# Kernel optimization log

Hardware: AMD Instinct MI355X
Metric: run time of the kernel (lower is better)

Reference implementation:

```python
import jax, jax.numpy as jnp
import numpy as np

MODEL_DIM = 1024
NUM_HEADS = 16
K_DIM = MODEL_DIM // NUM_HEADS


def setup_inputs() -> dict:
    key = jax.random.key(0)
    k1, k2, k3 = jax.random.split(key, 3)
    x = jax.random.normal(k1, (4, 2048, MODEL_DIM), dtype=jnp.float32)
    # nn.Linear(model_dim, 3*model_dim, bias=False): store as [D, 3D] so y = x @ W
    wqkv = jax.random.normal(k2, (MODEL_DIM, 3 * MODEL_DIM), dtype=jnp.float32) * (MODEL_DIM ** -0.5)
    wo = jax.random.normal(k3, (MODEL_DIM, MODEL_DIM), dtype=jnp.float32) * (MODEL_DIM ** -0.5)
    return {"x": x, "wqkv": wqkv, "wo": wo}


def reference(x, wqkv, wo):
    B, L, D = x.shape
    H, K = NUM_HEADS, K_DIM
    qkv = jnp.einsum("bld,de->ble", x, wqkv)  # [B, L, 3D]
    q, k, v = jnp.split(qkv, 3, axis=-1)
    # Faithful to source: plain reshape (no transpose) into [B, H, L, K]
    qh = q.reshape(B, H, L, K)
    kh = k.reshape(B, H, L, K)
    vh = v.reshape(B, H, L, K)
    scores = jnp.einsum("bhlk,bhmk->bhlm", qh, kh) / jnp.sqrt(jnp.float32(K))
    # Faithful quirk: softmax over dim=1 (head axis), as in the source
    probs = jax.nn.softmax(scores, axis=1)
    attended = jnp.einsum("bhlm,bhmk->bhlk", probs, vh)  # [B, H, L, K]
    concatted = attended.transpose(0, 2, 1, 3).reshape(B, L, D)
    return jnp.einsum("bld,de->ble", concatted, wo)
```

## Files before the change

### kernel.cpp

```cpp
#include <hip/hip_runtime.h>
#include <hip/hip_bf16.h>
#include <stdint.h>

typedef __attribute__((ext_vector_type(8))) short short8;
typedef __attribute__((ext_vector_type(4))) float floatx4;

#define QSCALE 0.18033688f

__device__ __forceinline__ unsigned short f2bf(float f) {
    unsigned int u = __float_as_uint(f);
    u += 0x7fffu + ((u >> 16) & 1u);
    return (unsigned short)(u >> 16);
}
__device__ __forceinline__ unsigned int pack2bf(float a, float b) {
    __hip_bfloat162 h = __float22bfloat162_rn(make_float2(a, b));
    return *reinterpret_cast<unsigned int*>(&h);
}

__device__ __forceinline__ void async16(const void* g, void* l) {
    __builtin_amdgcn_global_load_lds(
        (const __attribute__((address_space(1))) unsigned int*)g,
        (__attribute__((address_space(3))) unsigned int*)l, 16, 0, 0);
}

__global__ __launch_bounds__(256) void cvt_bf16(const float* __restrict__ src,
                                                unsigned short* __restrict__ dst, int n8) {
    int i = blockIdx.x * 256 + threadIdx.x;
    if (i >= n8) return;
    const float4 a = ((const float4*)src)[2 * i];
    const float4 b = ((const float4*)src)[2 * i + 1];
    ushort4 lo, hi;
    lo.x = f2bf(a.x); lo.y = f2bf(a.y); lo.z = f2bf(a.z); lo.w = f2bf(a.w);
    hi.x = f2bf(b.x); hi.y = f2bf(b.y); hi.z = f2bf(b.z); hi.w = f2bf(b.w);
    ((ushort4*)dst)[2 * i] = lo;
    ((ushort4*)dst)[2 * i + 1] = hi;
}

__global__ __launch_bounds__(256) void tcvt(const float* __restrict__ src,
                                            unsigned short* __restrict__ dst, int R, int C) {
    __shared__ unsigned short t[64][72];
    const int tid = threadIdx.x;
    const int r0 = blockIdx.y * 64, c0 = blockIdx.x * 64;
    #pragma unroll
    for (int it = 0; it < 4; it++) {
        int idx = it * 256 + tid;
        int rr = idx >> 4, cc = (idx & 15) * 4;
        float4 v = *(const float4*)(src + (size_t)(r0 + rr) * C + c0 + cc);
        t[cc + 0][rr] = f2bf(v.x);
        t[cc + 1][rr] = f2bf(v.y);
        t[cc + 2][rr] = f2bf(v.z);
        t[cc + 3][rr] = f2bf(v.w);
    }
    __syncthreads();
    #pragma unroll
    for (int it = 0; it < 2; it++) {
        int idx = it * 256 + tid;
        int cc = idx >> 3, r8 = (idx & 7) * 8;
        short8 v = *(const short8*)&t[cc][r8];
        *(short8*)(dst + (size_t)(c0 + cc) * R + r0 + r8) = v;
    }
}

__global__ __launch_bounds__(256) void vtrans(const unsigned short* __restrict__ vb,
                                              unsigned short* __restrict__ vbt) {
    __shared__ unsigned short t[64][72];
    const int tid = threadIdx.x;
    const int bh = blockIdx.y, m0 = blockIdx.x * 64;
    const unsigned short* src = vb + ((size_t)bh * 2048 + m0) * 64;
    unsigned short* dst = vbt + ((size_t)bh << 17) + m0;
    union { short8 v; unsigned short u[8]; } tmp;
    #pragma unroll
    for (int it = 0; it < 2; it++) {
        int idx = it * 256 + tid;
        int m = idx >> 3, c8 = (idx & 7) * 8;
        tmp.v = *(const short8*)(src + (size_t)m * 64 + c8);
        #pragma unroll
        for (int j = 0; j < 8; j++) t[c8 + j][m] = tmp.u[j];
    }
    __syncthreads();
    #pragma unroll
    for (int it = 0; it < 2; it++) {
        int idx = it * 256 + tid;
        int k = idx >> 3, c8 = (idx & 7) * 8;
        short8 v = *(const short8*)&t[k][c8];
        *(short8*)(dst + (size_t)k * 2048 + c8) = v;
    }
}

__global__ __launch_bounds__(256) void qkv_gemm(
    const unsigned short* __restrict__ A, const unsigned short* __restrict__ Bt,
    unsigned short* __restrict__ qb, unsigned short* __restrict__ kb,
    unsigned short* __restrict__ vb)
{
    __shared__ __align__(16) unsigned short As[128 * 32];
    __shared__ __align__(16) unsigned short Bs[128 * 32];
    const int tid = threadIdx.x, wave = tid >> 6, lane = tid & 63;
    const int quad = lane >> 4, lr = lane & 15;
    const int wr = wave >> 1, wc = wave & 1;
    const int bm = blockIdx.y * 128, bn = blockIdx.x * 128;
    const int lrow = lane >> 2, lcol = (lane & 3) * 8;

    floatx4 acc[4][4];
    #pragma unroll
    for (int i = 0; i < 4; i++)
        #pragma unroll
        for (int j = 0; j < 4; j++) acc[i][j] = (floatx4)0.0f;

    for (int k0 = 0; k0 < 1024; k0 += 32) {
        #pragma unroll
        for (int t = 0; t < 2; t++) {
            const int rbase = wave * 32 + t * 16;
            const int r = rbase + lrow;
            async16(A  + (size_t)(bm + r) * 1024 + k0 + lcol, &As[rbase * 32]);
            async16(Bt + (size_t)(bn + r) * 1024 + k0 + lcol, &Bs[rbase * 32]);
        }
        __syncthreads();
        short8 af[4], bfr[4];
        #pragma unroll
        for (int i = 0; i < 4; i++)
            af[i] = *(const short8*)&As[(wr * 64 + i * 16 + lr) * 32 + quad * 8];
        #pragma unroll
        for (int j = 0; j < 4; j++)
            bfr[j] = *(const short8*)&Bs[(wc * 64 + j * 16 + lr) * 32 + quad * 8];
        #pragma unroll
        for (int i = 0; i < 4; i++)
            #pragma unroll
            for (int j = 0; j < 4; j++)
                acc[i][j] = __builtin_amdgcn_mfma_f32_16x16x32_bf16(af[i], bfr[j], acc[i][j], 0, 0, 0);
        __syncthreads();
    }

    const int part = bn >> 10;
    unsigned short* __restrict__ dstb = (part == 0) ? qb : ((part == 1) ? kb : vb);
    const float sc = (part == 0) ? QSCALE : 1.0f;
    const int dbase = bn & 1023;
    #pragma unroll
    for (int i = 0; i < 4; i++)
        #pragma unroll
        for (int j = 0; j < 4; j++)
            #pragma unroll
            for (int r = 0; r < 4; r++) {
                int row = bm + wr * 64 + i * 16 + quad * 4 + r;
                int d   = dbase + wc * 64 + j * 16 + lr;
                int b = row >> 11, l = row & 2047;
                int flat = (l << 10) | d;
                int h = flat >> 17;
                int rem = flat & 131071;
                int l2 = rem >> 6, kk = rem & 63;
                dstb[((size_t)(b * 16 + h) * 2048 + l2) * 64 + kk] = f2bf(acc[i][j][r] * sc);
            }
}

__global__ __launch_bounds__(256) void out_gemm(
    const unsigned short* __restrict__ A, const unsigned short* __restrict__ Bt,
    float* __restrict__ C)
{
    __shared__ __align__(16) unsigned short As[128 * 32];
    __shared__ __align__(16) unsigned short Bs[128 * 32];
    const int tid = threadIdx.x, wave = tid >> 6, lane = tid & 63;
    const int quad = lane >> 4, lr = lane & 15;
    const int wr = wave >> 1, wc = wave & 1;
    const int bm = blockIdx.y * 128, bn = blockIdx.x * 128;
    const int lrow = lane >> 2, lcol = (lane & 3) * 8;

    floatx4 acc[4][4];
    #pragma unroll
    for (int i = 0; i < 4; i++)
        #pragma unroll
        for (int j = 0; j < 4; j++) acc[i][j] = (floatx4)0.0f;

    for (int k0 = 0; k0 < 1024; k0 += 32) {
        #pragma unroll
        for (int t = 0; t < 2; t++) {
            const int rbase = wave * 32 + t * 16;
            const int r = rbase + lrow;
            async16(A  + (size_t)(bm + r) * 1024 + k0 + lcol, &As[rbase * 32]);
            async16(Bt + (size_t)(bn + r) * 1024 + k0 + lcol, &Bs[rbase * 32]);
        }
        __syncthreads();
        short8 af[4], bfr[4];
        #pragma unroll
        for (int i = 0; i < 4; i++)
            af[i] = *(const short8*)&As[(wr * 64 + i * 16 + lr) * 32 + quad * 8];
        #pragma unroll
        for (int j = 0; j < 4; j++)
            bfr[j] = *(const short8*)&Bs[(wc * 64 + j * 16 + lr) * 32 + quad * 8];
        #pragma unroll
        for (int i = 0; i < 4; i++)
            #pragma unroll
            for (int j = 0; j < 4; j++)
                acc[i][j] = __builtin_amdgcn_mfma_f32_16x16x32_bf16(af[i], bfr[j], acc[i][j], 0, 0, 0);
        __syncthreads();
    }
    #pragma unroll
    for (int i = 0; i < 4; i++)
        #pragma unroll
        for (int j = 0; j < 4; j++)
            #pragma unroll
            for (int r = 0; r < 4; r++) {
                int row = bm + wr * 64 + i * 16 + quad * 4 + r;
                int col = bn + wc * 64 + j * 16 + lr;
                C[(size_t)row * 1024 + col] = acc[i][j][r];
            }
}

__global__ __launch_bounds__(256, 5) void attn_denom(
    const unsigned short* __restrict__ qb, const unsigned short* __restrict__ kb,
    unsigned short* __restrict__ drpT)
{
    __shared__ __align__(16) unsigned short Qs[2][64 * 64];
    __shared__ __align__(16) unsigned short Ks[2][64 * 64];
    const int tid = threadIdx.x, wave = tid >> 6, lane = tid & 63;
    const int quad = lane >> 4, lr = lane & 15;
    const int e7 = lr & 7;
    const int M0 = blockIdx.x * 64, L0 = blockIdx.y * 64, b = blockIdx.z;

    const int klr = lane >> 3;
    const int ksw8 = ((lane & 7) ^ klr) * 8;
    const size_t hb0 = ((size_t)(b * 16)) << 17;
    const unsigned short* qsrc0 = qb + hb0 + (size_t)(L0 + wave * 8 + klr) * 64 + ksw8;
    const unsigned short* ksrc0 = kb + hb0 + (size_t)(M0 + wave * 8 + klr) * 64 + ksw8;

    floatx4 e[4];
    #pragma unroll
    for (int i = 0; i < 4; i++) e[i] = (floatx4)0.0f;

    async16(qsrc0,           &Qs[0][(wave * 8) * 64]);
    async16(qsrc0 + 32 * 64, &Qs[0][(32 + wave * 8) * 64]);
    async16(ksrc0,           &Ks[0][(wave * 8) * 64]);
    async16(ksrc0 + 32 * 64, &Ks[0][(32 + wave * 8) * 64]);
    __syncthreads();

    for (int h = 0; h < 16; h++) {
        const int cur = h & 1, nxt = cur ^ 1;
        if (h < 15) {
            const unsigned short* qs = qsrc0 + ((size_t)(h + 1) << 17);
            const unsigned short* ks = ksrc0 + ((size_t)(h + 1) << 17);
            async16(qs,           &Qs[nxt][(wave * 8) * 64]);
            async16(qs + 32 * 64, &Qs[nxt][(32 + wave * 8) * 64]);
            async16(ks,           &Ks[nxt][(wave * 8) * 64]);
            async16(ks + 32 * 64, &Ks[nxt][(32 + wave * 8) * 64]);
        }
        const unsigned short* qsp = &Qs[cur][0];
        const unsigned short* ksp = &Ks[cur][0];
        const int rq = wave * 16 + lr;
        short8 qf0 = *(const short8*)&qsp[rq * 64 + (quad ^ e7) * 8];
        short8 qf1 = *(const short8*)&qsp[rq * 64 + ((4 + quad) ^ e7) * 8];
        #pragma unroll
        for (int mt = 0; mt < 4; mt++) {
            const int rk = mt * 16 + lr;
            short8 kf0 = *(const short8*)&ksp[rk * 64 + (quad ^ e7) * 8];
            short8 kf1 = *(const short8*)&ksp[rk * 64 + ((4 + quad) ^ e7) * 8];
            floatx4 s = (floatx4)0.0f;
            __builtin_amdgcn_s_setprio(1);
            s = __builtin_amdgcn_mfma_f32_16x16x32_bf16(kf0, qf0, s, 0, 0, 0);
            s = __builtin_amdgcn_mfma_f32_16x16x32_bf16(kf1, qf1, s, 0, 0, 0);
            __builtin_amdgcn_s_setprio(0);
            e[mt][0] += __builtin_amdgcn_exp2f(s[0]);
            e[mt][1] += __builtin_amdgcn_exp2f(s[1]);
            e[mt][2] += __builtin_amdgcn_exp2f(s[2]);
            e[mt][3] += __builtin_amdgcn_exp2f(s[3]);
        }
        if (h < 15) __syncthreads();
    }
    #pragma unroll
    for (int mt = 0; mt < 4; mt++) {
        float r0 = __builtin_amdgcn_rcpf(e[mt][0]);
        float r1 = __builtin_amdgcn_rcpf(e[mt][1]);
        float r2 = __builtin_amdgcn_rcpf(e[mt][2]);
        float r3 = __builtin_amdgcn_rcpf(e[mt][3]);
        uint2 o;
        o.x = pack2bf(r0, r1);
        o.y = pack2bf(r2, r3);
        int mtg = (M0 >> 4) + mt;
        int ltg = (L0 >> 4) + wave;
        *(uint2*)(drpT + ((((size_t)b * 128 + mtg) * 128 + ltg) << 8) + lane * 4) = o;
    }
}

__global__ __launch_bounds__(256, 4) void attn_pv(
    const unsigned short* __restrict__ qb, const unsigned short* __restrict__ kb,
    const unsigned short* __restrict__ vbt, const unsigned short* __restrict__ drpT,
    unsigned short* __restrict__ cb)
{
    __shared__ __align__(16) unsigned short KV[3][64 * 64];
    __shared__ __align__(16) unsigned short Ps[128 * 64];
    const int tid = threadIdx.x, wave = tid >> 6, lane = tid & 63;
    const int quad = lane >> 4, lr = lane & 15;
    const int e7 = lr & 7;
    const int flat = blockIdx.x;
    const int swz = (flat & 7) * 128 + (flat >> 3);
    const int Lt = swz & 15;
    const int h = (swz >> 4) & 15;
    const int b = swz >> 8;
    const int L0 = Lt * 128;
    const size_t head = (size_t)(b * 16 + h);
    const unsigned short* qbase = qb + (head << 17);
    const unsigned short* kbase = kb + (head << 17);
    const unsigned short* vtb   = vbt + (head << 17);
    const unsigned short* dbase = drpT + (((size_t)b * 128 * 128 + (L0 >> 4) + wave * 2) << 8) + lane * 4;

    const int klr = lane >> 3;
    const int ksw = (lane & 7) ^ klr;
    const unsigned short* ksrc0 = kbase + (size_t)(wave * 8 + klr) * 64 + ksw * 8;
    const unsigned short* vsrc0 = vtb + (size_t)(wave * 8 + klr) * 2048 + ksw * 8;

    short8 qf[2][2];
    #pragma unroll
    for (int j = 0; j < 2; j++) {
        const unsigned short* qr = qbase + (size_t)(L0 + wave * 32 + j * 16 + lr) * 64;
        qf[j][0] = *(const short8*)(qr + quad * 8);
        qf[j][1] = *(const short8*)(qr + 32 + quad * 8);
    }

    floatx4 oacc[2][4];
    #pragma unroll
    for (int i = 0; i < 2; i++)
        #pragma unroll
        for (int j = 0; j < 4; j++) oacc[i][j] = (floatx4)0.0f;

    async16(ksrc0,             &KV[0][(wave * 8) * 64]);
    async16(ksrc0 + 32 * 64,   &KV[0][(32 + wave * 8) * 64]);
    async16(vsrc0,             &KV[1][(wave * 8) * 64]);
    async16(vsrc0 + 32 * 2048, &KV[1][(32 + wave * 8) * 64]);
    uint2 du[4][2];
    #pragma unroll
    for (int mt = 0; mt < 4; mt++)
        #pragma unroll
        for (int j = 0; j < 2; j++)
            du[mt][j] = *(const uint2*)(dbase + ((size_t)mt << 15) + (j << 8));
    __syncthreads();

    int kcur = 0, vcur = 1, sp = 2;
    for (int t = 0; t < 32; t++) {
        const int M0 = t * 64;
        if (t < 31) {
            const unsigned short* ks = ksrc0 + (size_t)(M0 + 64) * 64;
            async16(ks,           &KV[sp][(wave * 8) * 64]);
            async16(ks + 32 * 64, &KV[sp][(32 + wave * 8) * 64]);
        }
        const unsigned short* ksp = &KV[kcur][0];
        #pragma unroll
        for (int mt = 0; mt < 4; mt++) {
            const int rk = mt * 16 + lr;
            short8 kf0 = *(const short8*)&ksp[rk * 64 + (quad ^ e7) * 8];
            short8 kf1 = *(const short8*)&ksp[rk * 64 + ((4 + quad) ^ e7) * 8];
            #pragma unroll
            for (int j = 0; j < 2; j++) {
                uint2 duv = du[mt][j];
                floatx4 s = (floatx4)0.0f;
                __builtin_amdgcn_s_setprio(1);
                s = __builtin_amdgcn_mfma_f32_16x16x32_bf16(kf0, qf[j][0], s, 0, 0, 0);
                s = __builtin_amdgcn_mfma_f32_16x16x32_bf16(kf1, qf[j][1], s, 0, 0, 0);
                __builtin_amdgcn_s_setprio(0);
                float r0 = __uint_as_float(duv.x << 16);
                float r1 = __uint_as_float(duv.x & 0xffff0000u);
                float r2 = __uint_as_float(duv.y << 16);
                float r3 = __uint_as_float(duv.y & 0xffff0000u);
                float p0 = __builtin_amdgcn_exp2f(s[0]) * r0;
                float p1 = __builtin_amdgcn_exp2f(s[1]) * r1;
                float p2 = __builtin_amdgcn_exp2f(s[2]) * r2;
                float p3 = __builtin_amdgcn_exp2f(s[3]) * r3;
                uint2 o;
                o.x = pack2bf(p0, p1);
                o.y = pack2bf(p2, p3);
                const int l_loc = wave * 32 + j * 16 + lr;
                const int lb16 = mt * 2 + (quad >> 1);
                *(uint2*)&Ps[l_loc * 64 + (lb16 ^ e7) * 8 + (quad & 1) * 4] = o;
            }
        }
        if (t < 31) {
            __syncthreads();
            const unsigned short* vs = vsrc0 + (M0 + 64);
            async16(vs,             &KV[kcur][(wave * 8) * 64]);
            async16(vs + 32 * 2048, &KV[kcur][(32 + wave * 8) * 64]);
            #pragma unroll
            for (int mt = 0; mt < 4; mt++)
                #pragma unroll
                for (int j = 0; j < 2; j++)
                    du[mt][j] = *(const uint2*)(dbase + (((size_t)((t + 1) * 4 + mt)) << 15) + (j << 8));
        }
        __builtin_amdgcn_sched_barrier(0);
        const unsigned short* vsp = &KV[vcur][0];
        #pragma unroll
        for (int f = 0; f < 2; f++) {
            short8 pf[2], vf[4];
            #pragma unroll
            for (int i2 = 0; i2 < 2; i2++)
                pf[i2] = *(const short8*)&Ps[(wave * 32 + i2 * 16 + lr) * 64 + ((f * 4 + quad) ^ e7) * 8];
            #pragma unroll
            for (int j2 = 0; j2 < 4; j2++) {
                const int rv = j2 * 16 + lr;
                vf[j2] = *(const short8*)&vsp[rv * 64 + ((f * 4 + quad) ^ e7) * 8];
            }
            __builtin_amdgcn_s_setprio(1);
            #pragma unroll
            for (int j2 = 0; j2 < 4; j2++)
                #pragma unroll
                for (int i2 = 0; i2 < 2; i2++)
                    oacc[i2][j2] = __builtin_amdgcn_mfma_f32_16x16x32_bf16(
                        pf[i2], vf[j2], oacc[i2][j2], 0, 0, 0);
            __builtin_amdgcn_s_setprio(0);
        }
        if (t < 31) {
            __syncthreads();
            const int ok = kcur;
            kcur = sp;
            sp = vcur;
            vcur = ok;
        }
    }
    #pragma unroll
    for (int i2 = 0; i2 < 2; i2++)
        #pragma unroll
        for (int j2 = 0; j2 < 4; j2++)
            #pragma unroll
            for (int r = 0; r < 4; r++) {
                int row = L0 + wave * 32 + i2 * 16 + quad * 4 + r;
                int col = h * 64 + j2 * 16 + lr;
                cb[(size_t)(b * 2048 + row) * 1024 + col] = f2bf(oacc[i2][j2][r]);
            }
}

extern "C" void kernel_launch(void* const* d_in, const int* in_sizes, int n_in,
                              void* d_out, int out_size, void* d_ws, size_t ws_size,
                              hipStream_t stream) {
    const float* x    = (const float*)d_in[0];
    const float* wqkv = (const float*)d_in[1];
    const float* wo   = (const float*)d_in[2];
    float* out = (float*)d_out;

    unsigned short* W = (unsigned short*)d_ws;
    unsigned short* qb   = W;
    unsigned short* kb   = W + 8388608;
    unsigned short* vbt  = W + 16777216;
    unsigned short* drpT = W + 25165824;
    unsigned short* cb   = W + 41943040;
    unsigned short* xb    = drpT;
    unsigned short* wqkvT = drpT + 8388608;
    unsigned short* vb    = cb;
    unsigned short* woT   = drpT;

    cvt_bf16  <<<4096, 256, 0, stream>>>(x, xb, 1048576);
    tcvt      <<<dim3(48, 16), 256, 0, stream>>>(wqkv, wqkvT, 1024, 3072);
    qkv_gemm  <<<dim3(24, 64), 256, 0, stream>>>(xb, wqkvT, qb, kb, vb);
    vtrans    <<<dim3(32, 64), 256, 0, stream>>>(vb, vbt);
    attn_denom<<<dim3(32, 32, 4), 256, 0, stream>>>(qb, kb, drpT);
    attn_pv   <<<1024, 256, 0, stream>>>(qb, kb, vbt, drpT, cb);
    tcvt      <<<dim3(16, 16), 256, 0, stream>>>(wo, woT, 1024, 1024);
    out_gemm  <<<dim3(8, 64), 256, 0, stream>>>(cb, woT, out);
}
```

Baseline: 353.7 us.

## Double-buffer LDS in projection GEMMs and swizzle block order

Both the QKV and output projection GEMMs now use two LDS buffers. The next K-slice is loaded asynchronously while MFMAs run on the current one, which removes one barrier per iteration. Block indices are remapped with an XCD-style swizzle (flat & 7) to improve L2 locality across chiplets. s_setprio is raised around the MFMA block. This doubles LDS use per block, which may reduce occupancy.

```diff
diff --git a/kernel.cpp b/kernel.cpp
--- a/kernel.cpp
+++ b/kernel.cpp
@@ -92,12 +92,14 @@
     unsigned short* __restrict__ qb, unsigned short* __restrict__ kb,
     unsigned short* __restrict__ vb)
 {
-    __shared__ __align__(16) unsigned short As[128 * 32];
-    __shared__ __align__(16) unsigned short Bs[128 * 32];
+    __shared__ __align__(16) unsigned short As[2][128 * 32];
+    __shared__ __align__(16) unsigned short Bs[2][128 * 32];
     const int tid = threadIdx.x, wave = tid >> 6, lane = tid & 63;
     const int quad = lane >> 4, lr = lane & 15;
     const int wr = wave >> 1, wc = wave & 1;
-    const int bm = blockIdx.y * 128, bn = blockIdx.x * 128;
+    const int flat = blockIdx.x;
+    const int swz = (flat & 7) * 192 + (flat >> 3);
+    const int bm = (swz / 24) * 128, bn = (swz % 24) * 128;
     const int lrow = lane >> 2, lcol = (lane & 3) * 8;
 
     floatx4 acc[4][4];
@@ -106,28 +108,42 @@
         #pragma unroll
         for (int j = 0; j < 4; j++) acc[i][j] = (floatx4)0.0f;
 
-    for (int k0 = 0; k0 < 1024; k0 += 32) {
-        #pragma unroll
-        for (int t = 0; t < 2; t++) {
-            const int rbase = wave * 32 + t * 16;
-            const int r = rbase + lrow;
-            async16(A  + (size_t)(bm + r) * 1024 + k0 + lcol, &As[rbase * 32]);
-            async16(Bt + (size_t)(bn + r) * 1024 + k0 + lcol, &Bs[rbase * 32]);
-        }
-        __syncthreads();
+    #pragma unroll
+    for (int t = 0; t < 2; t++) {
+        const int rbase = wave * 32 + t * 16;
+        const int r = rbase + lrow;
+        async16(A  + (size_t)(bm + r) * 1024 + lcol, &As[0][rbase * 32]);
+        async16(Bt + (size_t)(bn + r) * 1024 + lcol, &Bs[0][rbase * 32]);
+    }
+    __syncthreads();
+
+    for (int ks = 0; ks < 32; ks++) {
+        const int cur = ks & 1, nxt = cur ^ 1;
+        if (ks < 31) {
+            const int k0 = (ks + 1) * 32;
+            #pragma unroll
+            for (int t = 0; t < 2; t++) {
+                const int rbase = wave * 32 + t * 16;
+                const int r = rbase + lrow;
+                async16(A  + (size_t)(bm + r) * 1024 + k0 + lcol, &As[nxt][rbase * 32]);
+                async16(Bt + (size_t)(bn + r) * 1024 + k0 + lcol, &Bs[nxt][rbase * 32]);
+            }
+        }
         short8 af[4], bfr[4];
         #pragma unroll
         for (int i = 0; i < 4; i++)
-            af[i] = *(const short8*)&As[(wr * 64 + i * 16 + lr) * 32 + quad * 8];
+            af[i] = *(const short8*)&As[cur][(wr * 64 + i * 16 + lr) * 32 + quad * 8];
         #pragma unroll
         for (int j = 0; j < 4; j++)
-            bfr[j] = *(const short8*)&Bs[(wc * 64 + j * 16 + lr) * 32 + quad * 8];
+            bfr[j] = *(const short8*)&Bs[cur][(wc * 64 + j * 16 + lr) * 32 + quad * 8];
+        __builtin_amdgcn_s_setprio(1);
         #pragma unroll
         for (int i = 0; i < 4; i++)
             #pragma unroll
             for (int j = 0; j < 4; j++)
                 acc[i][j] = __builtin_amdgcn_mfma_f32_16x16x32_bf16(af[i], bfr[j], acc[i][j], 0, 0, 0);
-        __syncthreads();
+        __builtin_amdgcn_s_setprio(0);
+        if (ks < 31) __syncthreads();
     }
 
     const int part = bn >> 10;
@@ -143,9 +159,9 @@
                 int row = bm + wr * 64 + i * 16 + quad * 4 + r;
                 int d   = dbase + wc * 64 + j * 16 + lr;
                 int b = row >> 11, l = row & 2047;
-                int flat = (l << 10) | d;
-                int h = flat >> 17;
-                int rem = flat & 131071;
+                int flat2 = (l << 10) | d;
+                int h = flat2 >> 17;
+                int rem = flat2 & 131071;
                 int l2 = rem >> 6, kk = rem & 63;
                 dstb[((size_t)(b * 16 + h) * 2048 + l2) * 64 + kk] = f2bf(acc[i][j][r] * sc);
             }
@@ -155,12 +171,14 @@
     const unsigned short* __restrict__ A, const unsigned short* __restrict__ Bt,
     float* __restrict__ C)
 {
-    __shared__ __align__(16) unsigned short As[128 * 32];
-    __shared__ __align__(16) unsigned short Bs[128 * 32];
+    __shared__ __align__(16) unsigned short As[2][128 * 32];
+    __shared__ __align__(16) unsigned short Bs[2][128 * 32];
     const int tid = threadIdx.x, wave = tid >> 6, lane = tid & 63;
     const int quad = lane >> 4, lr = lane & 15;
     const int wr = wave >> 1, wc = wave & 1;
-    const int bm = blockIdx.y * 128, bn = blockIdx.x * 128;
+    const int flat = blockIdx.x;
+    const int swz = (flat & 7) * 64 + (flat >> 3);
+    const int bm = (swz >> 3) * 128, bn = (swz & 7) * 128;
     const int lrow = lane >> 2, lcol = (lane & 3) * 8;
 
     floatx4 acc[4][4];
@@ -169,28 +187,42 @@
         #pragma unroll
         for (int j = 0; j < 4; j++) acc[i][j] = (floatx4)0.0f;
 
-    for (int k0 = 0; k0 < 1024; k0 += 32) {
-        #pragma unroll
-        for (int t = 0; t < 2; t++) {
-            const int rbase = wave * 32 + t * 16;
-            const int r = rbase + lrow;
-            async16(A  + (size_t)(bm + r) * 1024 + k0 + lcol, &As[rbase * 32]);
-            async16(Bt + (size_t)(bn + r) * 1024 + k0 + lcol, &Bs[rbase * 32]);
-        }
-        __syncthreads();
+    #pragma unroll
+    for (int t = 0; t < 2; t++) {
+        const int rbase = wave * 32 + t * 16;
+        const int r = rbase + lrow;
+        async16(A  + (size_t)(bm + r) * 1024 + lcol, &As[0][rbase * 32]);
+        async16(Bt + (size_t)(bn + r) * 1024 + lcol, &Bs[0][rbase * 32]);
+    }
+    __syncthreads();
+
+    for (int ks = 0; ks < 32; ks++) {
+        const int cur = ks & 1, nxt = cur ^ 1;
+        if (ks < 31) {
+            const int k0 = (ks + 1) * 32;
+            #pragma unroll
+            for (int t = 0; t < 2; t++) {
+                const int rbase = wave * 32 + t * 16;
+                const int r = rbase + lrow;
+                async16(A  + (size_t)(bm + r) * 1024 + k0 + lcol, &As[nxt][rbase * 32]);
+                async16(Bt + (size_t)(bn + r) * 1024 + k0 + lcol, &Bs[nxt][rbase * 32]);
+            }
+        }
         short8 af[4], bfr[4];
         #pragma unroll
         for (int i = 0; i < 4; i++)
-            af[i] = *(const short8*)&As[(wr * 64 + i * 16 + lr) * 32 + quad * 8];
+            af[i] = *(const short8*)&As[cur][(wr * 64 + i * 16 + lr) * 32 + quad * 8];
         #pragma unroll
         for (int j = 0; j < 4; j++)
-            bfr[j] = *(const short8*)&Bs[(wc * 64 + j * 16 + lr) * 32 + quad * 8];
+            bfr[j] = *(const short8*)&Bs[cur][(wc * 64 + j * 16 + lr) * 32 + quad * 8];
+        __builtin_amdgcn_s_setprio(1);
         #pragma unroll
         for (int i = 0; i < 4; i++)
             #pragma unroll
             for (int j = 0; j < 4; j++)
                 acc[i][j] = __builtin_amdgcn_mfma_f32_16x16x32_bf16(af[i], bfr[j], acc[i][j], 0, 0, 0);
-        __syncthreads();
+        __builtin_amdgcn_s_setprio(0);
+        if (ks < 31) __syncthreads();
     }
     #pragma unroll
     for (int i = 0; i < 4; i++)
@@ -443,10 +475,10 @@
 
     cvt_bf16  <<<4096, 256, 0, stream>>>(x, xb, 1048576);
     tcvt      <<<dim3(48, 16), 256, 0, stream>>>(wqkv, wqkvT, 1024, 3072);
-    qkv_gemm  <<<dim3(24, 64), 256, 0, stream>>>(xb, wqkvT, qb, kb, vb);
+    qkv_gemm  <<<1536, 256, 0, stream>>>(xb, wqkvT, qb, kb, vb);
     vtrans    <<<dim3(32, 64), 256, 0, stream>>>(vb, vbt);
     attn_denom<<<dim3(32, 32, 4), 256, 0, stream>>>(qb, kb, drpT);
     attn_pv   <<<1024, 256, 0, stream>>>(qb, kb, vbt, drpT, cb);
     tcvt      <<<dim3(16, 16), 256, 0, stream>>>(wo, woT, 1024, 1024);
-    out_gemm  <<<dim3(8, 64), 256, 0, stream>>>(cb, woT, out);
-}
+    out_gemm  <<<512, 256, 0, stream>>>(cb, woT, out);
+}
```

Result: slower. 363.7 us (+2.8%).
